# Kernel tuning notes

Measured on AMD Instinct MI355X. Metric: run time of the kernel, lower is better.

Reference implementation:

```python
import jax, jax.numpy as jnp
import numpy as np
import math

L, N, Q, C, H = 6, 32, 100, 256, 8


def setup_inputs() -> dict:
    key = jax.random.key(0)
    k0, k1, k2 = jax.random.split(key, 3)
    hs_pair = jax.random.normal(k0, (L, N, Q, C), jnp.float32)
    xb = math.sqrt(6.0 / (C + 3 * C))  # xavier_uniform bound for (3C, C)
    in_proj_w = jax.random.uniform(k1, (3 * C, C), jnp.float32, -xb, xb)
    in_proj_b = jnp.zeros((3 * C,), jnp.float32)
    ob = 1.0 / math.sqrt(C)  # nn.Linear default bound
    out_w = jax.random.uniform(k2, (C, C), jnp.float32, -ob, ob)
    out_b = jnp.zeros((C,), jnp.float32)
    return {"hs_pair": hs_pair, "in_proj_w": in_proj_w, "in_proj_b": in_proj_b,
            "out_w": out_w, "out_b": out_b}


def _smha(q, k, v, ipw, ipb, ow, ob, mask=None):
    """Sigmoid multi-head attention (SMHA), batch-first.
    q: (N,T,E), k/v: (N,S,E), mask: (T,S) bool (True = masked -> attn 0).
    Returns (out (N,T,E), head-averaged pre-normalization sigmoid weights (N,T,S))."""
    E = q.shape[-1]
    Dh = E // H
    Nb, T, _ = q.shape
    S = k.shape[1]
    wq, wk, wv = ipw[:E], ipw[E:2 * E], ipw[2 * E:]
    bq, bk, bv = ipb[:E], ipb[E:2 * E], ipb[2 * E:]
    qh = (q @ wq.T + bq).reshape(Nb, T, H, Dh)
    kh = (k @ wk.T + bk).reshape(Nb, S, H, Dh)
    vh = (v @ wv.T + bv).reshape(Nb, S, H, Dh)
    scores = jnp.einsum('nthd,nshd->nhts', qh, kh) / jnp.sqrt(jnp.asarray(Dh, qh.dtype))
    attn = jax.nn.sigmoid(scores)
    if mask is not None:
        attn = jnp.where(mask[None, None], 0.0, attn)  # sigmoid(-inf) == 0
    out = jnp.einsum('nhts,nshd->nthd', attn / (attn.sum(-1, keepdims=True) + 1e-4), vh)
    out = out.reshape(Nb, T, E) @ ow.T + ob
    return out, attn.mean(axis=1)


def _sqdist(a, b):
    # a (...,M,C), b (...,K,C) -> squared euclidean (...,M,K); avoids (M,K,C) diff tensor
    return jnp.maximum(jnp.sum(a * a, -1)[..., :, None] + jnp.sum(b * b, -1)[..., None, :]
                       - 2.0 * jnp.einsum('...mc,...kc->...mk', a, b), 0.0)


def _forward(hs_pair, ipw, ipb, ow, ob):
    hs = hs_pair[-1]  # (N,Q,C)
    Nb = hs.shape[0]

    # mean_farthest_assignment over all layers: centers (L,N,2,C)
    c1_all = hs_pair.mean(2, keepdims=True)                      # (L,N,1,C)
    d_all = _sqdist(c1_all, hs_pair)[..., 0, :]                  # (L,N,Q); sq dist preserves argmax
    far_all = jnp.argmax(d_all, -1)
    c2_all = jnp.take_along_axis(hs_pair, far_all[..., None, None], axis=2)
    centers = jnp.concatenate([c1_all, c2_all], 2)               # (L,N,2,C)

    # global field: 2 centers attend to Q pair features
    mf, assignment = _smha(centers[-1], hs, hs, ipw, ipb, ow, ob)  # (N,2,C), (N,2,Q)
    card = assignment.sum(-1)                                      # (N,2)
    s_idx = jnp.argmin(card, -1)
    d_idx = jnp.argmax(card, -1)
    cd = jnp.take_along_axis(mf, d_idx[:, None, None], 1)[:, 0]    # (N,C)
    cs = jnp.take_along_axis(mf, s_idx[:, None, None], 1)[:, 0]

    # base_idx row j = (j..j+Q-2) mod Q, i.e. it excludes (j-1) mod Q
    excl = (jnp.arange(Q) - 1) % Q
    sum_all = hs.sum(1)                                            # (N,C)
    rows = jnp.arange(Q)

    def branch(kv, c1):
        # kv (N,S,C); c1 (N,Q,C) leave-one-out means; returns shift (N,Q)
        S = kv.shape[1]
        d = _sqdist(c1, kv)                                        # (N,Q,S)
        em = jnp.arange(S)[None, :] == excl[:, None]               # exclude col (j-1)%Q
        far = jnp.argmax(jnp.where(em[None], -jnp.inf, d), -1)     # (N,Q)
        c2 = jnp.take_along_axis(kv, far[..., None], axis=1)       # (N,Q,C)
        cen = jnp.stack([c1, c2], 2).reshape(Nb, 2 * Q, C)         # interleaved [c1_j, c2_j]
        m = jnp.zeros((2 * Q, S), bool).at[2 * rows, rows].set(True).at[2 * rows + 1, rows].set(True)
        mfx, asg = _smha(cen, kv, kv, ipw, ipb, ow, ob, mask=m)    # (N,2Q,C), (N,2Q,S)
        mfx = mfx.reshape(Nb, Q, 2, C)
        asg = asg.reshape(Nb, Q, 2, S)
        cardx = asg.sum(-1)                                        # (N,Q,2)
        si = jnp.argmin(cardx, -1)
        di = jnp.argmax(cardx, -1)
        cdx = jnp.take_along_axis(mfx, di[..., None, None], 2)[:, :, 0]  # (N,Q,C)
        csx = jnp.take_along_axis(mfx, si[..., None, None], 2)[:, :, 0]
        return (jnp.sqrt(jnp.sum((cdx - cd[:, None]) ** 2, -1) + 1e-12)
                + jnp.sqrt(jnp.sum((csx - cs[:, None]) ** 2, -1) + 1e-12))

    # remove-one branch
    c1_rm = (sum_all[:, None] - hs[:, excl]) / (Q - 1)
    shift_rm = branch(hs, c1_rm)

    # mean-displace branch: subset + batch-mean pseudo point appended
    mean_pair = hs.mean(1, keepdims=True)                          # (N,1,C)
    kv_md = jnp.concatenate([hs, mean_pair], 1)                    # (N,Q+1,C)
    c1_md = (sum_all[:, None] - hs[:, excl] + mean_pair) / Q
    shift_md = branch(kv_md, c1_md)

    return assignment, s_idx, d_idx, shift_rm, shift_md


def reference(hs_pair, in_proj_w, in_proj_b, out_w, out_b):
    return _forward(hs_pair, in_proj_w, in_proj_b, out_w, out_b)
```

## Files before the change

### kernel.cpp

```cpp
#include <hip/hip_runtime.h>
#include <math.h>

#define NB 32
#define QQ 100
#define CC 256
#define HH 8
#define DH 32
#define SM 101
#define TT 200
#define TB 400
#define PW 768

typedef __attribute__((ext_vector_type(8))) short s16x8;
typedef __attribute__((ext_vector_type(4))) float f32x4;

__device__ inline ushort2 tsplit(float x) {
    unsigned u = __float_as_uint(x);
    float l = x - __uint_as_float(u & 0xffff0000u);
    ushort2 r;
    r.x = (unsigned short)(u >> 16);
    r.y = (unsigned short)(__float_as_uint(l) >> 16);
    return r;
}
__device__ inline unsigned short f2bf(float x) {
    unsigned u = __float_as_uint(x);
    return (unsigned short)((u + 0x7fffu + ((u >> 16) & 1u)) >> 16);
}

__global__ __launch_bounds__(256)
void meanrow_kernel(const float* __restrict__ hs, float* __restrict__ meanF) {
    int n = blockIdx.x, cb = blockIdx.y;
    int tid = threadIdx.x;
    int c = cb * 128 + (tid & 127), rh = tid >> 7;
    __shared__ float part[2][128];
    const float* h = hs + (size_t)n * QQ * CC;
    float s = 0.f;
    for (int q = rh * 50; q < rh * 50 + 50; ++q) s += h[(size_t)q * CC + c];
    part[rh][tid & 127] = s;
    __syncthreads();
    if (rh == 0) meanF[(size_t)n * CC + c] = (part[0][tid & 127] + part[1][tid & 127]) * 0.01f;
}

#define LDK 40
__global__ __launch_bounds__(256, 2)
void gemm_mfma(const float* __restrict__ hs, const float* __restrict__ meanF,
               const float* __restrict__ W_g, const float* __restrict__ bias,
               float* __restrict__ out, int M, int Nout) {
    __shared__ unsigned short Ahs[128][LDK], Als[128][LDK], Bhs[128][LDK], Bls[128][LDK];
    int tid = threadIdx.x;
    int lane = tid & 63, wave = tid >> 6;
    int wm = (wave >> 1) * 64, wn = (wave & 1) * 64;
    int fr = lane & 15, kb = lane >> 4;
    int bm = blockIdx.x * 128, bn = blockIdx.y * 128;
    int srow = tid >> 1, scol = (tid & 1) * 16;
    int am = bm + srow; if (am >= M) am = M - 1;
    int an = am / SM, ar = am - an * SM;
    const float* pA = (ar < QQ) ? hs + ((size_t)an * QQ + ar) * CC + scol
                                : meanF + (size_t)an * CC + scol;
    const float* pW = W_g + (size_t)(bn + srow) * CC + scol;
    f32x4 acc[4][4];
#pragma unroll
    for (int mi = 0; mi < 4; ++mi)
#pragma unroll
        for (int ni = 0; ni < 4; ++ni)
            acc[mi][ni] = (f32x4){0.f, 0.f, 0.f, 0.f};
    for (int k0 = 0; k0 < CC; k0 += 32) {
        float4 av[4], wv[4];
#pragma unroll
        for (int j = 0; j < 4; ++j) {
            av[j] = *(const float4*)(pA + k0 + 4 * j);
            wv[j] = *(const float4*)(pW + k0 + 4 * j);
        }
        __syncthreads();
#pragma unroll
        for (int j = 0; j < 4; ++j) {
            ushort2 sx = tsplit(av[j].x), sy = tsplit(av[j].y), sz = tsplit(av[j].z), sw = tsplit(av[j].w);
            ushort4 h4; h4.x = sx.x; h4.y = sy.x; h4.z = sz.x; h4.w = sw.x;
            ushort4 l4; l4.x = sx.y; l4.y = sy.y; l4.z = sz.y; l4.w = sw.y;
            *(ushort4*)&Ahs[srow][scol + 4 * j] = h4;
            *(ushort4*)&Als[srow][scol + 4 * j] = l4;
            ushort2 tx = tsplit(wv[j].x), ty = tsplit(wv[j].y), tz = tsplit(wv[j].z), tw = tsplit(wv[j].w);
            ushort4 wh4; wh4.x = tx.x; wh4.y = ty.x; wh4.z = tz.x; wh4.w = tw.x;
            ushort4 wl4; wl4.x = tx.y; wl4.y = ty.y; wl4.z = tz.y; wl4.w = tw.y;
            *(ushort4*)&Bhs[srow][scol + 4 * j] = wh4;
            *(ushort4*)&Bls[srow][scol + 4 * j] = wl4;
        }
        __syncthreads();
        s16x8 fah[4], fal[4], fbh[4], fbl[4];
#pragma unroll
        for (int mi = 0; mi < 4; ++mi) {
            fah[mi] = *(const s16x8*)&Ahs[wm + mi * 16 + fr][kb * 8];
            fal[mi] = *(const s16x8*)&Als[wm + mi * 16 + fr][kb * 8];
        }
#pragma unroll
        for (int ni = 0; ni < 4; ++ni) {
            fbh[ni] = *(const s16x8*)&Bhs[wn + ni * 16 + fr][kb * 8];
            fbl[ni] = *(const s16x8*)&Bls[wn + ni * 16 + fr][kb * 8];
        }
#pragma unroll
        for (int mi = 0; mi < 4; ++mi)
#pragma unroll
            for (int ni = 0; ni < 4; ++ni) {
                acc[mi][ni] = __builtin_amdgcn_mfma_f32_16x16x32_bf16(fah[mi], fbh[ni], acc[mi][ni], 0, 0, 0);
                acc[mi][ni] = __builtin_amdgcn_mfma_f32_16x16x32_bf16(fah[mi], fbl[ni], acc[mi][ni], 0, 0, 0);
                acc[mi][ni] = __builtin_amdgcn_mfma_f32_16x16x32_bf16(fal[mi], fbh[ni], acc[mi][ni], 0, 0, 0);
            }
    }
#pragma unroll
    for (int mi = 0; mi < 4; ++mi) {
        int mb = bm + wm + mi * 16 + kb * 4;
#pragma unroll
        for (int r = 0; r < 4; ++r) {
            int m = mb + r;
            if (m < M) {
#pragma unroll
                for (int ni = 0; ni < 4; ++ni) {
                    int col = bn + wn + ni * 16 + fr;
                    out[(size_t)m * Nout + col] = acc[mi][ni][r] + bias[col];
                }
            }
        }
    }
}

__global__ __launch_bounds__(256, 2)
void gram_strip(const float* __restrict__ hs, const float* __restrict__ meanF,
                float* __restrict__ G) {
    int ti = blockIdx.x, n = blockIdx.y;
    int tid = threadIdx.x;
    int wave = tid >> 6, lane = tid & 63;
    int fr = lane & 15, kb = lane >> 4;
    __shared__ unsigned short Ah[112][LDK], Al[112][LDK];
    const float* hb = hs + (size_t)n * QQ * CC;
    const float* mb = meanF + (size_t)n * CC;
    f32x4 acc[2];
    acc[0] = (f32x4){0.f, 0.f, 0.f, 0.f};
    acc[1] = (f32x4){0.f, 0.f, 0.f, 0.f};
    int tj0 = wave, tj1 = wave + 4;
    for (int k0 = 0; k0 < CC; k0 += 32) {
        __syncthreads();
        if (tid < 224) {
            int row = tid >> 1, kk = (tid & 1) * 16;
            float4 v[4];
            if (row < SM) {
                const float* rp = (row < QQ) ? hb + (size_t)row * CC : mb;
#pragma unroll
                for (int j = 0; j < 4; ++j) v[j] = *(const float4*)(rp + k0 + kk + 4 * j);
            } else {
#pragma unroll
                for (int j = 0; j < 4; ++j) v[j] = (float4){0.f, 0.f, 0.f, 0.f};
            }
#pragma unroll
            for (int j = 0; j < 4; ++j) {
                ushort2 sx = tsplit(v[j].x), sy = tsplit(v[j].y), sz = tsplit(v[j].z), sw = tsplit(v[j].w);
                ushort4 h4; h4.x = sx.x; h4.y = sy.x; h4.z = sz.x; h4.w = sw.x;
                ushort4 l4; l4.x = sx.y; l4.y = sy.y; l4.z = sz.y; l4.w = sw.y;
                *(ushort4*)&Ah[row][kk + 4 * j] = h4;
                *(ushort4*)&Al[row][kk + 4 * j] = l4;
            }
        }
        __syncthreads();
        s16x8 ah = *(const s16x8*)&Ah[ti * 16 + fr][kb * 8];
        s16x8 al = *(const s16x8*)&Al[ti * 16 + fr][kb * 8];
        {
            s16x8 bh = *(const s16x8*)&Ah[tj0 * 16 + fr][kb * 8];
            s16x8 bl = *(const s16x8*)&Al[tj0 * 16 + fr][kb * 8];
            acc[0] = __builtin_amdgcn_mfma_f32_16x16x32_bf16(ah, bh, acc[0], 0, 0, 0);
            acc[0] = __builtin_amdgcn_mfma_f32_16x16x32_bf16(ah, bl, acc[0], 0, 0, 0);
            acc[0] = __builtin_amdgcn_mfma_f32_16x16x32_bf16(al, bh, acc[0], 0, 0, 0);
        }
        if (tj1 < 7) {
            s16x8 bh = *(const s16x8*)&Ah[tj1 * 16 + fr][kb * 8];
            s16x8 bl = *(const s16x8*)&Al[tj1 * 16 + fr][kb * 8];
            acc[1] = __builtin_amdgcn_mfma_f32_16x16x32_bf16(ah, bh, acc[1], 0, 0, 0);
            acc[1] = __builtin_amdgcn_mfma_f32_16x16x32_bf16(ah, bl, acc[1], 0, 0, 0);
            acc[1] = __builtin_amdgcn_mfma_f32_16x16x32_bf16(al, bh, acc[1], 0, 0, 0);
        }
    }
    float* Gn = G + (size_t)n * SM * 104;
#pragma unroll
    for (int u = 0; u < 2; ++u) {
        int tj = u ? tj1 : tj0;
        if (tj >= 7) continue;
#pragma unroll
        for (int r = 0; r < 4; ++r) {
            int m = ti * 16 + kb * 4 + r;
            int col = tj * 16 + fr;
            if (m < SM && col < SM) Gn[(size_t)m * 104 + col] = (u ? acc[1] : acc[0])[r];
        }
    }
}

__global__ __launch_bounds__(256)
void farsel(const float* __restrict__ G, const float* __restrict__ P_all,
            float* __restrict__ Psum0, int* __restrict__ far0,
            int* __restrict__ far_rm, int* __restrict__ far_md) {
    int n = blockIdx.x;
    int tid = threadIdx.x;
    __shared__ float sumdot[104], meandot[104], norm[104];
    const float* Gn = G + (size_t)n * SM * 104;
    {
        const float* basep = P_all + (size_t)n * SM * PW + tid;
        float accp = 0.f;
        for (int q = 0; q < QQ; ++q) accp += basep[(size_t)q * PW];
        Psum0[(size_t)n * CC + tid] = accp;
    }
    if (tid < SM) {
        const float* row = Gn + (size_t)tid * 104;
        float a = 0.f;
        for (int q = 0; q < QQ; ++q) a += row[q];
        sumdot[tid] = a; meandot[tid] = row[QQ]; norm[tid] = row[tid];
    }
    __syncthreads();
    if (tid < QQ) {
        int q = tid, qm1 = (q + QQ - 1) % QQ;
        const float* gq = Gn + (size_t)qm1 * 104;
        int best = -1; float bv = -1e30f;
        for (int s = 0; s < QQ; ++s) {
            if (s == qm1) continue;
            float val = norm[s] - (sumdot[s] - gq[s]) * (2.f / 99.f);
            if (val > bv) { bv = val; best = s; }
        }
        far_rm[n * QQ + q] = best;
    } else if (tid >= 128 && tid < 128 + QQ) {
        int q = tid - 128, qm1 = (q + QQ - 1) % QQ;
        const float* gq = Gn + (size_t)qm1 * 104;
        int best = -1; float bv = -1e30f;
        for (int s = 0; s < SM; ++s) {
            if (s == qm1) continue;
            float val = norm[s] - (sumdot[s] - gq[s] + meandot[s]) * (2.f / 100.f);
            if (val > bv) { bv = val; best = s; }
        }
        far_md[n * QQ + q] = best;
    } else if (tid == 100) {
        int best = 0; float bv = -1e30f;
        for (int q = 0; q < QQ; ++q) {
            float val = norm[q] - 0.02f * sumdot[q];
            if (val > bv) { bv = val; best = q; }
        }
        far0[n] = best;
    }
}

__global__ __launch_bounds__(512)
void smhaB_kernel(const float* __restrict__ P_all, const int* __restrict__ far0,
                  const float* __restrict__ ow, const float* __restrict__ ob,
                  float* __restrict__ out_assign, float* __restrict__ out_sidx,
                  float* __restrict__ out_didx, float* __restrict__ cd,
                  float* __restrict__ cs) {
    int n = blockIdx.x;
    int tid = threadIdx.x;
    int h = tid >> 6, lane = tid & 63;
    __shared__ float at[HH][2][104];
    __shared__ float qsh[HH][2][DH];
    __shared__ float rsh[HH][2];
    __shared__ float pvs[2][CC];
    __shared__ int sdi[2];
    const float* base = P_all + (size_t)n * SM * PW;
    if (lane < 2 * DH) {
        int t = lane >> 5, d = lane & 31;
        int row = t ? far0[n] : QQ;
        qsh[h][t][d] = base[(size_t)row * PW + h * DH + d];
    }
    const float scl = 0.17677669529663687f;
    float p0 = 0.f, p1 = 0.f;
    for (int s = lane; s < 104; s += 64) {
        float a0v = 0.f, a1v = 0.f;
        if (s < QQ) {
            const float4* kr = (const float4*)(base + (size_t)s * PW + CC + h * DH);
            float d0 = 0.f, d1 = 0.f;
#pragma unroll
            for (int j = 0; j < 8; ++j) {
                float4 k4 = kr[j];
                d0 += qsh[h][0][4 * j] * k4.x + qsh[h][0][4 * j + 1] * k4.y
                    + qsh[h][0][4 * j + 2] * k4.z + qsh[h][0][4 * j + 3] * k4.w;
                d1 += qsh[h][1][4 * j] * k4.x + qsh[h][1][4 * j + 1] * k4.y
                    + qsh[h][1][4 * j + 2] * k4.z + qsh[h][1][4 * j + 3] * k4.w;
            }
            a0v = 1.f / (1.f + __expf(-d0 * scl));
            a1v = 1.f / (1.f + __expf(-d1 * scl));
            p0 += a0v; p1 += a1v;
        }
        at[h][0][s] = a0v;
        at[h][1][s] = a1v;
    }
#pragma unroll
    for (int off = 32; off > 0; off >>= 1) {
        p0 += __shfl_down(p0, off);
        p1 += __shfl_down(p1, off);
    }
    if (lane == 0) { rsh[h][0] = p0; rsh[h][1] = p1; }
    {
        int t = lane >> 5, d = lane & 31;
        float rv = (t ? p1 : p0);
        rv = __shfl(rv, 0);
        float inv = 1.f / (rv + 1e-4f);
        float acc = 0.f;
        const float* vb = base + 2 * CC + h * DH + d;
        for (int s = 0; s < QQ; ++s) acc += at[h][t][s] * vb[(size_t)s * PW];
        pvs[t][h * DH + d] = acc * inv;
    }
    __syncthreads();
    if (tid == 0) {
        float c0 = 0.f, c1v = 0.f;
        for (int h2 = 0; h2 < HH; ++h2) { c0 += rsh[h2][0]; c1v += rsh[h2][1]; }
        int si = (c1v < c0) ? 1 : 0;
        int di = (c1v > c0) ? 1 : 0;
        sdi[0] = si; sdi[1] = di;
        out_sidx[n] = (float)si;
        out_didx[n] = (float)di;
    }
    __syncthreads();
    if (tid < 2 * QQ) {
        int t = tid / QQ, s = tid % QQ;
        float m = 0.f;
#pragma unroll
        for (int h2 = 0; h2 < HH; ++h2) m += at[h2][t][s];
        out_assign[(size_t)n * 2 * QQ + tid] = m * 0.125f;
    }
    {
        int t = tid >> 8, c = tid & 255;
        const float4* wr4 = (const float4*)(ow + (size_t)c * CC);
        const float4* pz = (const float4*)&pvs[t][0];
        float a = ob[c];
#pragma unroll 8
        for (int k = 0; k < 64; ++k) {
            float4 w = wr4[k], x = pz[k];
            a += x.x * w.x + x.y * w.y + x.z * w.z + x.w * w.w;
        }
        if (t == sdi[1]) cd[(size_t)n * CC + c] = a;
        if (t == sdi[0]) cs[(size_t)n * CC + c] = a;
    }
}

__global__ __launch_bounds__(512)
void attn_mfma(const float* __restrict__ P_all, const float* __restrict__ Psum0,
               const int* __restrict__ far_rm, const int* __restrict__ far_md,
               float* __restrict__ pv, float* __restrict__ rowsum) {
    int h = blockIdx.x, n = blockIdx.y;
    int tid = threadIdx.x;
    int w = tid >> 6, lane = tid & 63;
    int fr = lane & 15, hi = lane >> 4;
    int d0 = hi * 8;
    __shared__ unsigned short Kh[112 * 40];
    __shared__ unsigned short Kl[112 * 40];
    __shared__ unsigned short Vt[32 * 136];
    __shared__ unsigned short Pb[8][64 * 40];
    __shared__ float rsL[8][64];
    const float* base = P_all + (size_t)n * SM * PW;
    for (int idx = tid; idx < 112 * 8; idx += 512) {
        int key = idx >> 3, d4 = (idx & 7) * 4;
        float4 kv = {0.f, 0.f, 0.f, 0.f}, vv = {0.f, 0.f, 0.f, 0.f};
        if (key < SM) {
            kv = *(const float4*)&base[(size_t)key * PW + CC + h * DH + d4];
            vv = *(const float4*)&base[(size_t)key * PW + 2 * CC + h * DH + d4];
        }
        ushort2 sx = tsplit(kv.x), sy = tsplit(kv.y), sz = tsplit(kv.z), sw = tsplit(kv.w);
        ushort4 h4; h4.x = sx.x; h4.y = sy.x; h4.z = sz.x; h4.w = sw.x;
        ushort4 l4; l4.x = sx.y; l4.y = sy.y; l4.z = sz.y; l4.w = sw.y;
        *(ushort4*)&Kh[key * 40 + d4] = h4;
        *(ushort4*)&Kl[key * 40 + d4] = l4;
        Vt[(d4 + 0) * 136 + key] = f2bf(vv.x);
        Vt[(d4 + 1) * 136 + key] = f2bf(vv.y);
        Vt[(d4 + 2) * 136 + key] = f2bf(vv.z);
        Vt[(d4 + 3) * 136 + key] = f2bf(vv.w);
    }
    for (int idx = tid; idx < 32 * 16; idx += 512) {
        int d = idx >> 4, key = 112 + (idx & 15);
        Vt[d * 136 + key] = 0;
    }
    __syncthreads();
    const float* Psum0n = Psum0 + n * CC;
    int rowbase = w * 50;
    unsigned short* Pw = Pb[w];
    const float scl = 0.17677669529663687f;
    s16x8 qh[4], ql[4];
    int mk[4], sb[4];
#pragma unroll
    for (int qi = 0; qi < 4; ++qi) {
        int lq = qi * 16 + fr;
        int row = rowbase + (lq < 50 ? lq : 49);
        int b = row >= TT;
        int t = row - b * TT;
        int q = t >> 1;
        mk[qi] = q; sb[qi] = b ? SM : QQ;
        float qv[8];
        if (t & 1) {
            int f = (b ? far_md : far_rm)[n * QQ + q];
            const float4* pr = (const float4*)(base + (size_t)f * PW + h * DH + d0);
            float4 v0 = pr[0], v1 = pr[1];
            qv[0] = v0.x; qv[1] = v0.y; qv[2] = v0.z; qv[3] = v0.w;
            qv[4] = v1.x; qv[5] = v1.y; qv[6] = v1.z; qv[7] = v1.w;
        } else {
            int qm1 = (q + QQ - 1) % QQ;
            const float4* ps = (const float4*)(Psum0n + h * DH + d0);
            const float4* pm = (const float4*)(base + (size_t)qm1 * PW + h * DH + d0);
            const float4* pmn = (const float4*)(base + (size_t)QQ * PW + h * DH + d0);
            float invd = b ? 0.01f : (1.f / 99.f);
            float bb = b ? 1.f : 0.f;
            float4 a0 = ps[0], c0 = pm[0], m0 = pmn[0];
            float4 a1 = ps[1], c1 = pm[1], m1 = pmn[1];
            qv[0] = (a0.x - c0.x + bb * m0.x) * invd;
            qv[1] = (a0.y - c0.y + bb * m0.y) * invd;
            qv[2] = (a0.z - c0.z + bb * m0.z) * invd;
            qv[3] = (a0.w - c0.w + bb * m0.w) * invd;
            qv[4] = (a1.x - c1.x + bb * m1.x) * invd;
            qv[5] = (a1.y - c1.y + bb * m1.y) * invd;
            qv[6] = (a1.z - c1.z + bb * m1.z) * invd;
            qv[7] = (a1.w - c1.w + bb * m1.w) * invd;
        }
        s16x8 qhv, qlv;
#pragma unroll
        for (int j = 0; j < 8; ++j) {
            ushort2 sp = tsplit(qv[j]);
            qhv[j] = (short)sp.x;
            qlv[j] = (short)sp.y;
        }
        qh[qi] = qhv; ql[qi] = qlv;
    }
    f32x4 pvacc[4][2];
#pragma unroll
    for (int qi = 0; qi < 4; ++qi) {
        pvacc[qi][0] = (f32x4){0.f, 0.f, 0.f, 0.f};
        pvacc[qi][1] = (f32x4){0.f, 0.f, 0.f, 0.f};
    }
    float rs[4] = {0.f, 0.f, 0.f, 0.f};
#pragma unroll
    for (int kc = 0; kc < 4; ++kc) {
        int k0 = kc * 32;
        {
            s16x8 ah = *(const s16x8*)&Kh[(k0 + fr) * 40 + d0];
            s16x8 al = *(const s16x8*)&Kl[(k0 + fr) * 40 + d0];
#pragma unroll
            for (int qi = 0; qi < 4; ++qi) {
                f32x4 s0 = (f32x4){0.f, 0.f, 0.f, 0.f};
                s0 = __builtin_amdgcn_mfma_f32_16x16x32_bf16(ah, qh[qi], s0, 0, 0, 0);
                s0 = __builtin_amdgcn_mfma_f32_16x16x32_bf16(ah, ql[qi], s0, 0, 0, 0);
                s0 = __builtin_amdgcn_mfma_f32_16x16x32_bf16(al, qh[qi], s0, 0, 0, 0);
                int kb0 = k0 + 4 * hi;
                float a0 = (kb0 + 0 < sb[qi] && kb0 + 0 != mk[qi]) ? 1.f / (1.f + __expf(-s0[0] * scl)) : 0.f;
                float a1 = (kb0 + 1 < sb[qi] && kb0 + 1 != mk[qi]) ? 1.f / (1.f + __expf(-s0[1] * scl)) : 0.f;
                float a2 = (kb0 + 2 < sb[qi] && kb0 + 2 != mk[qi]) ? 1.f / (1.f + __expf(-s0[2] * scl)) : 0.f;
                float a3 = (kb0 + 3 < sb[qi] && kb0 + 3 != mk[qi]) ? 1.f / (1.f + __expf(-s0[3] * scl)) : 0.f;
                rs[qi] += a0 + a1 + a2 + a3;
                ushort4 p4;
                p4.x = f2bf(a0); p4.y = f2bf(a1); p4.z = f2bf(a2); p4.w = f2bf(a3);
                *(ushort4*)&Pw[(qi * 16 + fr) * 40 + 4 * hi] = p4;
// ... 63 lines not shown
    }
}

__global__ __launch_bounds__(512)
void outshift(const float* __restrict__ pv, const float* __restrict__ ow,
              const float* __restrict__ ob, const float* __restrict__ cd,
              const float* __restrict__ cs, const float* __restrict__ rowsum,
              float* __restrict__ out_srm, float* __restrict__ out_smd) {
    __shared__ unsigned short Ahs[64][LDK], Als[64][LDK];
    __shared__ unsigned short Bhs[256][LDK], Bls[256][LDK];
    __shared__ float redcd[64][8], redcs[64][8];
    int tid = threadIdx.x;
    int lane = tid & 63, wave = tid >> 6;
    int wn = wave * 32;
    int fr = lane & 15, kb = lane >> 4;
    int bm = blockIdx.x * 64;
    int arow = tid >> 3, ak = (tid & 7) * 4;
    int brow = tid >> 1, bk = (tid & 1) * 16;
    const float* pA = pv + (size_t)(bm + arow) * CC + ak;
    const float* pB = ow + (size_t)brow * CC + bk;
    f32x4 acc[4][2];
#pragma unroll
    for (int mi = 0; mi < 4; ++mi)
#pragma unroll
        for (int ni = 0; ni < 2; ++ni)
            acc[mi][ni] = (f32x4){0.f, 0.f, 0.f, 0.f};
    for (int k0 = 0; k0 < CC; k0 += 32) {
        float4 av = *(const float4*)(pA + k0);
        float4 wv[4];
#pragma unroll
        for (int j = 0; j < 4; ++j) wv[j] = *(const float4*)(pB + k0 + 4 * j);
        __syncthreads();
        {
            ushort2 sx = tsplit(av.x), sy = tsplit(av.y), sz = tsplit(av.z), sw = tsplit(av.w);
            ushort4 h4; h4.x = sx.x; h4.y = sy.x; h4.z = sz.x; h4.w = sw.x;
            ushort4 l4; l4.x = sx.y; l4.y = sy.y; l4.z = sz.y; l4.w = sw.y;
            *(ushort4*)&Ahs[arow][ak] = h4;
            *(ushort4*)&Als[arow][ak] = l4;
        }
#pragma unroll
        for (int j = 0; j < 4; ++j) {
            ushort2 sx = tsplit(wv[j].x), sy = tsplit(wv[j].y), sz = tsplit(wv[j].z), sw = tsplit(wv[j].w);
            ushort4 h4; h4.x = sx.x; h4.y = sy.x; h4.z = sz.x; h4.w = sw.x;
            ushort4 l4; l4.x = sx.y; l4.y = sy.y; l4.z = sz.y; l4.w = sw.y;
            *(ushort4*)&Bhs[brow][bk + 4 * j] = h4;
            *(ushort4*)&Bls[brow][bk + 4 * j] = l4;
        }
        __syncthreads();
        s16x8 fah[4], fal[4], fbh[2], fbl[2];
#pragma unroll
        for (int mi = 0; mi < 4; ++mi) {
            fah[mi] = *(const s16x8*)&Ahs[mi * 16 + fr][kb * 8];
            fal[mi] = *(const s16x8*)&Als[mi * 16 + fr][kb * 8];
        }
#pragma unroll
        for (int ni = 0; ni < 2; ++ni) {
            fbh[ni] = *(const s16x8*)&Bhs[wn + ni * 16 + fr][kb * 8];
            fbl[ni] = *(const s16x8*)&Bls[wn + ni * 16 + fr][kb * 8];
        }
#pragma unroll
        for (int mi = 0; mi < 4; ++mi)
#pragma unroll
            for (int ni = 0; ni < 2; ++ni) {
                acc[mi][ni] = __builtin_amdgcn_mfma_f32_16x16x32_bf16(fah[mi], fbh[ni], acc[mi][ni], 0, 0, 0);
                acc[mi][ni] = __builtin_amdgcn_mfma_f32_16x16x32_bf16(fah[mi], fbl[ni], acc[mi][ni], 0, 0, 0);
                acc[mi][ni] = __builtin_amdgcn_mfma_f32_16x16x32_bf16(fal[mi], fbh[ni], acc[mi][ni], 0, 0, 0);
            }
    }
#pragma unroll
    for (int mi = 0; mi < 4; ++mi) {
#pragma unroll
        for (int r = 0; r < 4; ++r) {
            int lm = mi * 16 + kb * 4 + r;
            int g = bm + lm;
            int n = g / TB;
// ... 43 lines not shown

extern "C" void kernel_launch(void* const* d_in, const int* in_sizes, int n_in,
                              void* d_out, int out_size, void* d_ws, size_t ws_size,
                              hipStream_t stream) {
    const float* hs_pair = (const float*)d_in[0];
    const float* ipw = (const float*)d_in[1];
    const float* ipb = (const float*)d_in[2];
    const float* ow  = (const float*)d_in[3];
    const float* ob  = (const float*)d_in[4];
    const float* hs = hs_pair + (size_t)5 * NB * QQ * CC;

    float* ws = (float*)d_ws;
    size_t o = 0;
    float* meanF   = ws + o; o += NB * CC;
    float* P_all   = ws + o; o += (size_t)NB * SM * PW;
    float* Psum0   = ws + o; o += NB * CC;
    float* G       = ws + o; o += (size_t)NB * SM * 104;
    int*   far0    = (int*)(ws + o); o += NB;
    int*   far_rm  = (int*)(ws + o); o += NB * QQ;
    int*   far_md  = (int*)(ws + o); o += NB * QQ;
    float* cd      = ws + o; o += NB * CC;
    float* cs      = ws + o; o += NB * CC;
    float* pv      = ws + o; o += (size_t)NB * TB * CC;
    float* rowsum  = ws + o; o += (size_t)NB * HH * TB;
    if (o * sizeof(float) > ws_size) return;

    float* out = (float*)d_out;
    float* out_assign = out;
    float* out_sidx   = out + 6400;
    float* out_didx   = out + 6432;
    float* out_srm    = out + 6464;
    float* out_smd    = out + 9664;

    meanrow_kernel<<<dim3(NB, 2), 256, 0, stream>>>(hs, meanF);
    gemm_mfma<<<dim3((NB * SM + 127) / 128, PW / 128), 256, 0, stream>>>(
        hs, meanF, ipw, ipb, P_all, NB * SM, PW);
    gram_strip<<<dim3(7, NB), 256, 0, stream>>>(hs, meanF, G);
    farsel<<<NB, 256, 0, stream>>>(G, P_all, Psum0, far0, far_rm, far_md);
    smhaB_kernel<<<NB, 512, 0, stream>>>(P_all, far0, ow, ob, out_assign,
                                         out_sidx, out_didx, cd, cs);
    attn_mfma<<<dim3(HH, NB), 512, 0, stream>>>(P_all, Psum0, far_rm, far_md, pv, rowsum);
    outshift<<<NB * TB / 64, 512, 0, stream>>>(pv, ow, ob, cd, cs, rowsum, out_srm, out_smd);
}
```

Baseline: 116.8 us.

## Merge projection and Gram kernels, compute far0 in mean kernel, co-launch selection

The mean kernel now also computes the farthest point from the mean directly, so far0 no longer depends on the Gram matrix. The projection GEMM and Gram-strip kernels become one launch that dispatches on block index, and the far-point selection runs in the same launch as the SMHA-B block work. This cuts the launch count from seven to five and lets independent work run concurrently. The bf16 hi/lo split also switches from truncation to round-to-nearest, which changes numerics slightly.

```diff
diff --git a/kernel.cpp b/kernel.cpp
--- a/kernel.cpp
+++ b/kernel.cpp
@@ -14,322 +14,340 @@
 typedef __attribute__((ext_vector_type(8))) short s16x8;
 typedef __attribute__((ext_vector_type(4))) float f32x4;
 
-__device__ inline ushort2 tsplit(float x) {
-    unsigned u = __float_as_uint(x);
-    float l = x - __uint_as_float(u & 0xffff0000u);
-    ushort2 r;
-    r.x = (unsigned short)(u >> 16);
-    r.y = (unsigned short)(__float_as_uint(l) >> 16);
-    return r;
-}
 __device__ inline unsigned short f2bf(float x) {
     unsigned u = __float_as_uint(x);
     return (unsigned short)((u + 0x7fffu + ((u >> 16) & 1u)) >> 16);
 }
+__device__ inline float bf2f(unsigned short h) {
+    return __uint_as_float(((unsigned)h) << 16);
+}
+__device__ inline ushort2 rsplit(float x) {
+    ushort2 r;
+    r.x = f2bf(x);
+    r.y = f2bf(x - bf2f(r.x));
+    return r;
+}
 
 __global__ __launch_bounds__(256)
-void meanrow_kernel(const float* __restrict__ hs, float* __restrict__ meanF) {
-    int n = blockIdx.x, cb = blockIdx.y;
-    int tid = threadIdx.x;
-    int c = cb * 128 + (tid & 127), rh = tid >> 7;
-    __shared__ float part[2][128];
+void meanfar0(const float* __restrict__ hs, float* __restrict__ meanF,
+              int* __restrict__ far0) {
+    int n = blockIdx.x;
+    int c = threadIdx.x;
     const float* h = hs + (size_t)n * QQ * CC;
     float s = 0.f;
-    for (int q = rh * 50; q < rh * 50 + 50; ++q) s += h[(size_t)q * CC + c];
-    part[rh][tid & 127] = s;
+    for (int q = 0; q < QQ; ++q) s += h[q * CC + c];
+    float c1 = s * 0.01f;
+    meanF[(size_t)n * CC + c] = c1;
+    __shared__ float c1s[CC];
+    __shared__ float dls[QQ];
+    c1s[c] = c1;
     __syncthreads();
-    if (rh == 0) meanF[(size_t)n * CC + c] = (part[0][tid & 127] + part[1][tid & 127]) * 0.01f;
+    int wave = c >> 6, lane = c & 63;
+    for (int q = wave; q < QQ; q += 4) {
+        float p = 0.f;
+        for (int cc = lane; cc < CC; cc += 64) {
+            float d = c1s[cc] - h[q * CC + cc];
+            p += d * d;
+        }
+        for (int off = 32; off > 0; off >>= 1) p += __shfl_down(p, off);
+        if (lane == 0) dls[q] = p;
+    }
+    __syncthreads();
+    if (c == 0) {
+        int best = 0; float bv = dls[0];
+        for (int q = 1; q < QQ; ++q) if (dls[q] > bv) { bv = dls[q]; best = q; }
+        far0[n] = best;
+    }
 }
 
 #define LDK 40
+#define GEMM_BX 26
+#define GEMM_BY 6
+#define GEMM_NBLK (GEMM_BX * GEMM_BY)
 __global__ __launch_bounds__(256, 2)
-void gemm_mfma(const float* __restrict__ hs, const float* __restrict__ meanF,
-               const float* __restrict__ W_g, const float* __restrict__ bias,
-               float* __restrict__ out, int M, int Nout) {
-    __shared__ unsigned short Ahs[128][LDK], Als[128][LDK], Bhs[128][LDK], Bls[128][LDK];
+void projgram(const float* __restrict__ hs, const float* __restrict__ meanF,
+              const float* __restrict__ W_g, const float* __restrict__ bias,
+              float* __restrict__ out, float* __restrict__ G) {
+    __shared__ unsigned short u16buf[4 * 128 * LDK];
     int tid = threadIdx.x;
     int lane = tid & 63, wave = tid >> 6;
-    int wm = (wave >> 1) * 64, wn = (wave & 1) * 64;
     int fr = lane & 15, kb = lane >> 4;
-    int bm = blockIdx.x * 128, bn = blockIdx.y * 128;
-    int srow = tid >> 1, scol = (tid & 1) * 16;
-    int am = bm + srow; if (am >= M) am = M - 1;
-    int an = am / SM, ar = am - an * SM;
-    const float* pA = (ar < QQ) ? hs + ((size_t)an * QQ + ar) * CC + scol
-                                : meanF + (size_t)an * CC + scol;
-    const float* pW = W_g + (size_t)(bn + srow) * CC + scol;
-    f32x4 acc[4][4];
-#pragma unroll
-    for (int mi = 0; mi < 4; ++mi)
-#pragma unroll
-        for (int ni = 0; ni < 4; ++ni)
-            acc[mi][ni] = (f32x4){0.f, 0.f, 0.f, 0.f};
-    for (int k0 = 0; k0 < CC; k0 += 32) {
-        float4 av[4], wv[4];
-#pragma unroll
-        for (int j = 0; j < 4; ++j) {
-            av[j] = *(const float4*)(pA + k0 + 4 * j);
-            wv[j] = *(const float4*)(pW + k0 + 4 * j);
-        }
-        __syncthreads();
-#pragma unroll
-        for (int j = 0; j < 4; ++j) {
-            ushort2 sx = tsplit(av[j].x), sy = tsplit(av[j].y), sz = tsplit(av[j].z), sw = tsplit(av[j].w);
-            ushort4 h4; h4.x = sx.x; h4.y = sy.x; h4.z = sz.x; h4.w = sw.x;
-            ushort4 l4; l4.x = sx.y; l4.y = sy.y; l4.z = sz.y; l4.w = sw.y;
-            *(ushort4*)&Ahs[srow][scol + 4 * j] = h4;
-            *(ushort4*)&Als[srow][scol + 4 * j] = l4;
-            ushort2 tx = tsplit(wv[j].x), ty = tsplit(wv[j].y), tz = tsplit(wv[j].z), tw = tsplit(wv[j].w);
-            ushort4 wh4; wh4.x = tx.x; wh4.y = ty.x; wh4.z = tz.x; wh4.w = tw.x;
-            ushort4 wl4; wl4.x = tx.y; wl4.y = ty.y; wl4.z = tz.y; wl4.w = tw.y;
-            *(ushort4*)&Bhs[srow][scol + 4 * j] = wh4;
-            *(ushort4*)&Bls[srow][scol + 4 * j] = wl4;
-        }
-        __syncthreads();
-        s16x8 fah[4], fal[4], fbh[4], fbl[4];
-#pragma unroll
-        for (int mi = 0; mi < 4; ++mi) {
-            fah[mi] = *(const s16x8*)&Ahs[wm + mi * 16 + fr][kb * 8];
-            fal[mi] = *(const s16x8*)&Als[wm + mi * 16 + fr][kb * 8];
-        }
-#pragma unroll
-        for (int ni = 0; ni < 4; ++ni) {
-            fbh[ni] = *(const s16x8*)&Bhs[wn + ni * 16 + fr][kb * 8];
-            fbl[ni] = *(const s16x8*)&Bls[wn + ni * 16 + fr][kb * 8];
-        }
+    if (blockIdx.x < GEMM_NBLK) {
+        unsigned short* Ahs = u16buf;
+        unsigned short* Als = u16buf + 128 * LDK;
+        unsigned short* Bhs = u16buf + 2 * 128 * LDK;
+        unsigned short* Bls = u16buf + 3 * 128 * LDK;
+        const int M = NB * SM;
+        int bm = (blockIdx.x % GEMM_BX) * 128, bn = (blockIdx.x / GEMM_BX) * 128;
+        int wm = (wave >> 1) * 64, wn = (wave & 1) * 64;
+        int srow = tid >> 1, scol = (tid & 1) * 16;
+        int am = bm + srow; if (am >= M) am = M - 1;
+        int an = am / SM, ar = am - an * SM;
+        const float* pA = (ar < QQ) ? hs + ((size_t)an * QQ + ar) * CC + scol
+                                    : meanF + (size_t)an * CC + scol;
+        const float* pW = W_g + (size_t)(bn + srow) * CC + scol;
+        f32x4 acc[4][4];
 #pragma unroll
         for (int mi = 0; mi < 4; ++mi)
 #pragma unroll
-            for (int ni = 0; ni < 4; ++ni) {
-                acc[mi][ni] = __builtin_amdgcn_mfma_f32_16x16x32_bf16(fah[mi], fbh[ni], acc[mi][ni], 0, 0, 0);
-                acc[mi][ni] = __builtin_amdgcn_mfma_f32_16x16x32_bf16(fah[mi], fbl[ni], acc[mi][ni], 0, 0, 0);
-                acc[mi][ni] = __builtin_amdgcn_mfma_f32_16x16x32_bf16(fal[mi], fbh[ni], acc[mi][ni], 0, 0, 0);
-            }
-    }
-#pragma unroll
-    for (int mi = 0; mi < 4; ++mi) {
-        int mb = bm + wm + mi * 16 + kb * 4;
-#pragma unroll
-        for (int r = 0; r < 4; ++r) {
-            int m = mb + r;
-            if (m < M) {
-#pragma unroll
-                for (int ni = 0; ni < 4; ++ni) {
-                    int col = bn + wn + ni * 16 + fr;
-                    out[(size_t)m * Nout + col] = acc[mi][ni][r] + bias[col];
-                }
-            }
-        }
-    }
-}
-
-__global__ __launch_bounds__(256, 2)
-void gram_strip(const float* __restrict__ hs, const float* __restrict__ meanF,
-                float* __restrict__ G) {
-    int ti = blockIdx.x, n = blockIdx.y;
-    int tid = threadIdx.x;
-    int wave = tid >> 6, lane = tid & 63;
-    int fr = lane & 15, kb = lane >> 4;
-    __shared__ unsigned short Ah[112][LDK], Al[112][LDK];
-    const float* hb = hs + (size_t)n * QQ * CC;
-    const float* mb = meanF + (size_t)n * CC;
-    f32x4 acc[2];
-    acc[0] = (f32x4){0.f, 0.f, 0.f, 0.f};
-    acc[1] = (f32x4){0.f, 0.f, 0.f, 0.f};
-    int tj0 = wave, tj1 = wave + 4;
-    for (int k0 = 0; k0 < CC; k0 += 32) {
-        __syncthreads();
-        if (tid < 224) {
-            int row = tid >> 1, kk = (tid & 1) * 16;
-            float4 v[4];
-            if (row < SM) {
-                const float* rp = (row < QQ) ? hb + (size_t)row * CC : mb;
-#pragma unroll
-                for (int j = 0; j < 4; ++j) v[j] = *(const float4*)(rp + k0 + kk + 4 * j);
-            } else {
-#pragma unroll
-                for (int j = 0; j < 4; ++j) v[j] = (float4){0.f, 0.f, 0.f, 0.f};
-            }
+            for (int ni = 0; ni < 4; ++ni)
+                acc[mi][ni] = (f32x4){0.f, 0.f, 0.f, 0.f};
+        for (int k0 = 0; k0 < CC; k0 += 32) {
+            float4 av[4], wv[4];
 #pragma unroll
             for (int j = 0; j < 4; ++j) {
-                ushort2 sx = tsplit(v[j].x), sy = tsplit(v[j].y), sz = tsplit(v[j].z), sw = tsplit(v[j].w);
+                av[j] = *(const float4*)(pA + k0 + 4 * j);
+                wv[j] = *(const float4*)(pW + k0 + 4 * j);
+            }
+            __syncthreads();
+#pragma unroll
+            for (int j = 0; j < 4; ++j) {
+                ushort2 sx = rsplit(av[j].x), sy = rsplit(av[j].y), sz = rsplit(av[j].z), sw = rsplit(av[j].w);
                 ushort4 h4; h4.x = sx.x; h4.y = sy.x; h4.z = sz.x; h4.w = sw.x;
                 ushort4 l4; l4.x = sx.y; l4.y = sy.y; l4.z = sz.y; l4.w = sw.y;
-                *(ushort4*)&Ah[row][kk + 4 * j] = h4;
-                *(ushort4*)&Al[row][kk + 4 * j] = l4;
-            }
+                *(ushort4*)&Ahs[srow * LDK + scol + 4 * j] = h4;
+                *(ushort4*)&Als[srow * LDK + scol + 4 * j] = l4;
+                ushort2 tx = rsplit(wv[j].x), ty = rsplit(wv[j].y), tz = rsplit(wv[j].z), tw = rsplit(wv[j].w);
+                ushort4 wh4; wh4.x = tx.x; wh4.y = ty.x; wh4.z = tz.x; wh4.w = tw.x;
+                ushort4 wl4; wl4.x = tx.y; wl4.y = ty.y; wl4.z = tz.y; wl4.w = tw.y;
+                *(ushort4*)&Bhs[srow * LDK + scol + 4 * j] = wh4;
+                *(ushort4*)&Bls[srow * LDK + scol + 4 * j] = wl4;
+            }
+            __syncthreads();
+            s16x8 fah[4], fal[4], fbh[4], fbl[4];
+#pragma unroll
+            for (int mi = 0; mi < 4; ++mi) {
+                fah[mi] = *(const s16x8*)&Ahs[(wm + mi * 16 + fr) * LDK + kb * 8];
+                fal[mi] = *(const s16x8*)&Als[(wm + mi * 16 + fr) * LDK + kb * 8];
+            }
+#pragma unroll
+            for (int ni = 0; ni < 4; ++ni) {
+                fbh[ni] = *(const s16x8*)&Bhs[(wn + ni * 16 + fr) * LDK + kb * 8];
+                fbl[ni] = *(const s16x8*)&Bls[(wn + ni * 16 + fr) * LDK + kb * 8];
+            }
+#pragma unroll
+            for (int mi = 0; mi < 4; ++mi)
+#pragma unroll
+                for (int ni = 0; ni < 4; ++ni) {
+                    acc[mi][ni] = __builtin_amdgcn_mfma_f32_16x16x32_bf16(fah[mi], fbh[ni], acc[mi][ni], 0, 0, 0);
+                    acc[mi][ni] = __builtin_amdgcn_mfma_f32_16x16x32_bf16(fah[mi], fbl[ni], acc[mi][ni], 0, 0, 0);
+                    acc[mi][ni] = __builtin_amdgcn_mfma_f32_16x16x32_bf16(fal[mi], fbh[ni], acc[mi][ni], 0, 0, 0);
+                }
+        }
+#pragma unroll
+        for (int mi = 0; mi < 4; ++mi) {
+            int mb = bm + wm + mi * 16 + kb * 4;
+#pragma unroll
+            for (int r = 0; r < 4; ++r) {
+                int m = mb + r;
+                if (m < M) {
+#pragma unroll
+                    for (int ni = 0; ni < 4; ++ni) {
+                        int col = bn + wn + ni * 16 + fr;
+                        out[(size_t)m * PW + col] = acc[mi][ni][r] + bias[col];
+                    }
+                }
+            }
+        }
+    } else {
+        int bi = blockIdx.x - GEMM_NBLK;
+        int ti = bi % 7, n = bi / 7;
+        unsigned short* Ah = u16buf;
+        unsigned short* Al = u16buf + 112 * LDK;
+        const float* hb = hs + (size_t)n * QQ * CC;
+        const float* mb = meanF + (size_t)n * CC;
+        f32x4 acc[2];
+        acc[0] = (f32x4){0.f, 0.f, 0.f, 0.f};
+        acc[1] = (f32x4){0.f, 0.f, 0.f, 0.f};
+        int tj0 = wave, tj1 = wave + 4;
+        for (int k0 = 0; k0 < CC; k0 += 32) {
+            __syncthreads();
+            if (tid < 224) {
+                int row = tid >> 1, kk = (tid & 1) * 16;
+                float4 v[4];
+                if (row < SM) {
+                    const float* rp = (row < QQ) ? hb + (size_t)row * CC : mb;
+#pragma unroll
+                    for (int j = 0; j < 4; ++j) v[j] = *(const float4*)(rp + k0 + kk + 4 * j);
+                } else {
+#pragma unroll
+                    for (int j = 0; j < 4; ++j) v[j] = (float4){0.f, 0.f, 0.f, 0.f};
+                }
+#pragma unroll
+                for (int j = 0; j < 4; ++j) {
+                    ushort2 sx = rsplit(v[j].x), sy = rsplit(v[j].y), sz = rsplit(v[j].z), sw = rsplit(v[j].w);
+                    ushort4 h4; h4.x = sx.x; h4.y = sy.x; h4.z = sz.x; h4.w = sw.x;
+                    ushort4 l4; l4.x = sx.y; l4.y = sy.y; l4.z = sz.y; l4.w = sw.y;
+                    *(ushort4*)&Ah[row * LDK + kk + 4 * j] = h4;
+                    *(ushort4*)&Al[row * LDK + kk + 4 * j] = l4;
+                }
+            }
+            __syncthreads();
+            s16x8 ah = *(const s16x8*)&Ah[(ti * 16 + fr) * LDK + kb * 8];
+            s16x8 al = *(const s16x8*)&Al[(ti * 16 + fr) * LDK + kb * 8];
+            {
+                s16x8 bh = *(const s16x8*)&Ah[(tj0 * 16 + fr) * LDK + kb * 8];
+                s16x8 bl = *(const s16x8*)&Al[(tj0 * 16 + fr) * LDK + kb * 8];
+                acc[0] = __builtin_amdgcn_mfma_f32_16x16x32_bf16(ah, bh, acc[0], 0, 0, 0);
+                acc[0] = __builtin_amdgcn_mfma_f32_16x16x32_bf16(ah, bl, acc[0], 0, 0, 0);
+                acc[0] = __builtin_amdgcn_mfma_f32_16x16x32_bf16(al, bh, acc[0], 0, 0, 0);
+            }
+            if (tj1 < 7) {
+                s16x8 bh = *(const s16x8*)&Ah[(tj1 * 16 + fr) * LDK + kb * 8];
+                s16x8 bl = *(const s16x8*)&Al[(tj1 * 16 + fr) * LDK + kb * 8];
+                acc[1] = __builtin_amdgcn_mfma_f32_16x16x32_bf16(ah, bh, acc[1], 0, 0, 0);
+                acc[1] = __builtin_amdgcn_mfma_f32_16x16x32_bf16(ah, bl, acc[1], 0, 0, 0);
+                acc[1] = __builtin_amdgcn_mfma_f32_16x16x32_bf16(al, bh, acc[1], 0, 0, 0);
+            }
+        }
+        float* Gn = G + (size_t)n * SM * 104;
+#pragma unroll
+        for (int u = 0; u < 2; ++u) {
+            int tj = u ? tj1 : tj0;
+            if (tj >= 7) continue;
+#pragma unroll
+            for (int r = 0; r < 4; ++r) {
+                int m = ti * 16 + kb * 4 + r;
+                int col = tj * 16 + fr;
+                if (m < SM && col < SM) Gn[(size_t)m * 104 + col] = (u ? acc[1] : acc[0])[r];
+            }
+        }
+    }
+}
+
+__global__ __launch_bounds__(512)
+void selB(const float* __restrict__ G, const float* __restrict__ P_all,
+          const int* __restrict__ far0, const float* __restrict__ ow,
+          const float* __restrict__ ob, float* __restrict__ Psum0,
+          int* __restrict__ far_rm, int* __restrict__ far_md,
+          float* __restrict__ out_assign, float* __restrict__ out_sidx,
+          float* __restrict__ out_didx, float* __restrict__ cd,
+          float* __restrict__ cs) {
+    int tid = threadIdx.x;
+    if (blockIdx.x < NB) {
+        int n = blockIdx.x;
+        __shared__ float sumdot[104], meandot[104], norm[104];
+        __shared__ float psumP[2][CC];
+        const float* Gn = G + (size_t)n * SM * 104;
+        {
+            int c = tid & 255, half = tid >> 8;
+            const float* basep = P_all + (size_t)n * SM * PW + c;
+            float accp = 0.f;
+            for (int q = half * 50; q < half * 50 + 50; ++q) accp += basep[(size_t)q * PW];
+            psumP[half][c] = accp;
+        }
+        if (tid < SM) {
+            const float* row = Gn + (size_t)tid * 104;
+            float a = 0.f;
+            for (int q = 0; q < QQ; ++q) a += row[q];
+            sumdot[tid] = a; meandot[tid] = row[QQ]; norm[tid] = row[tid];
         }
         __syncthreads();
-        s16x8 ah = *(const s16x8*)&Ah[ti * 16 + fr][kb * 8];
-        s16x8 al = *(const s16x8*)&Al[ti * 16 + fr][kb * 8];
+        if (tid < 256) Psum0[(size_t)n * CC + tid] = psumP[0][tid] + psumP[1][tid];
+        if (tid < QQ) {
+            int q = tid, qm1 = (q + QQ - 1) % QQ;
+            const float* gq = Gn + (size_t)qm1 * 104;
+            int best = -1; float bv = -1e30f;
+            for (int s = 0; s < QQ; ++s) {
+                if (s == qm1) continue;
+                float val = norm[s] - (sumdot[s] - gq[s]) * (2.f / 99.f);
+                if (val > bv) { bv = val; best = s; }
+            }
+            far_rm[n * QQ + q] = best;
+        } else if (tid >= 128 && tid < 128 + QQ) {
+            int q = tid - 128, qm1 = (q + QQ - 1) % QQ;
+            const float* gq = Gn + (size_t)qm1 * 104;
+            int best = -1; float bv = -1e30f;
+            for (int s = 0; s < SM; ++s) {
+                if (s == qm1) continue;
+                float val = norm[s] - (sumdot[s] - gq[s] + meandot[s]) * (2.f / 100.f);
+                if (val > bv) { bv = val; best = s; }
+            }
+            far_md[n * QQ + q] = best;
+        }
+    } else {
+        int n = blockIdx.x - NB;
+        int h = tid >> 6, lane = tid & 63;
+        __shared__ float at[HH][2][104];
+        __shared__ float qsh[HH][2][DH];
+        __shared__ float rsh[HH][2];
+        __shared__ float pvs[2][CC];
+        __shared__ int sdi[2];
+        const float* base = P_all + (size_t)n * SM * PW;
+        if (lane < 2 * DH) {
+            int t = lane >> 5, d = lane & 31;
+            int row = t ? far0[n] : QQ;
+            qsh[h][t][d] = base[(size_t)row * PW + h * DH + d];
+        }
+        const float scl = 0.17677669529663687f;
+        float p0 = 0.f, p1 = 0.f;
+        for (int s = lane; s < 104; s += 64) {
+            float a0v = 0.f, a1v = 0.f;
+            if (s < QQ) {
+                const float4* kr = (const float4*)(base + (size_t)s * PW + CC + h * DH);
+                float d0 = 0.f, d1 = 0.f;
+#pragma unroll
+                for (int j = 0; j < 8; ++j) {
+                    float4 k4 = kr[j];
+                    d0 += qsh[h][0][4 * j] * k4.x + qsh[h][0][4 * j + 1] * k4.y
+                        + qsh[h][0][4 * j + 2] * k4.z + qsh[h][0][4 * j + 3] * k4.w;
+                    d1 += qsh[h][1][4 * j] * k4.x + qsh[h][1][4 * j + 1] * k4.y
+                        + qsh[h][1][4 * j + 2] * k4.z + qsh[h][1][4 * j + 3] * k4.w;
+                }
+                a0v = 1.f / (1.f + __expf(-d0 * scl));
+                a1v = 1.f / (1.f + __expf(-d1 * scl));
+                p0 += a0v; p1 += a1v;
+            }
+            at[h][0][s] = a0v;
+            at[h][1][s] = a1v;
+        }
+#pragma unroll
+        for (int off = 32; off > 0; off >>= 1) {
+            p0 += __shfl_down(p0, off);
+            p1 += __shfl_down(p1, off);
+        }
+        if (lane == 0) { rsh[h][0] = p0; rsh[h][1] = p1; }
         {
-            s16x8 bh = *(const s16x8*)&Ah[tj0 * 16 + fr][kb * 8];
-            s16x8 bl = *(const s16x8*)&Al[tj0 * 16 + fr][kb * 8];
-            acc[0] = __builtin_amdgcn_mfma_f32_16x16x32_bf16(ah, bh, acc[0], 0, 0, 0);
-            acc[0] = __builtin_amdgcn_mfma_f32_16x16x32_bf16(ah, bl, acc[0], 0, 0, 0);
-            acc[0] = __builtin_amdgcn_mfma_f32_16x16x32_bf16(al, bh, acc[0], 0, 0, 0);
-        }
-        if (tj1 < 7) {
-            s16x8 bh = *(const s16x8*)&Ah[tj1 * 16 + fr][kb * 8];
-            s16x8 bl = *(const s16x8*)&Al[tj1 * 16 + fr][kb * 8];
-            acc[1] = __builtin_amdgcn_mfma_f32_16x16x32_bf16(ah, bh, acc[1], 0, 0, 0);
-            acc[1] = __builtin_amdgcn_mfma_f32_16x16x32_bf16(ah, bl, acc[1], 0, 0, 0);
-            acc[1] = __builtin_amdgcn_mfma_f32_16x16x32_bf16(al, bh, acc[1], 0, 0, 0);
-        }
-    }
-    float* Gn = G + (size_t)n * SM * 104;
-#pragma unroll
-    for (int u = 0; u < 2; ++u) {
-        int tj = u ? tj1 : tj0;
-        if (tj >= 7) continue;
-#pragma unroll
-        for (int r = 0; r < 4; ++r) {
-            int m = ti * 16 + kb * 4 + r;
-            int col = tj * 16 + fr;
-            if (m < SM && col < SM) Gn[(size_t)m * 104 + col] = (u ? acc[1] : acc[0])[r];
-        }
-    }
-}
-
-__global__ __launch_bounds__(256)
-void farsel(const float* __restrict__ G, const float* __restrict__ P_all,
-            float* __restrict__ Psum0, int* __restrict__ far0,
-            int* __restrict__ far_rm, int* __restrict__ far_md) {
-    int n = blockIdx.x;
-    int tid = threadIdx.x;
-    __shared__ float sumdot[104], meandot[104], norm[104];
-    const float* Gn = G + (size_t)n * SM * 104;
-    {
-        const float* basep = P_all + (size_t)n * SM * PW + tid;
-        float accp = 0.f;
-        for (int q = 0; q < QQ; ++q) accp += basep[(size_t)q * PW];
-        Psum0[(size_t)n * CC + tid] = accp;
-    }
-    if (tid < SM) {
-        const float* row = Gn + (size_t)tid * 104;
-        float a = 0.f;
-        for (int q = 0; q < QQ; ++q) a += row[q];
-        sumdot[tid] = a; meandot[tid] = row[QQ]; norm[tid] = row[tid];
-    }
-    __syncthreads();
-    if (tid < QQ) {
-        int q = tid, qm1 = (q + QQ - 1) % QQ;
-        const float* gq = Gn + (size_t)qm1 * 104;
-        int best = -1; float bv = -1e30f;
-        for (int s = 0; s < QQ; ++s) {
-            if (s == qm1) continue;
-            float val = norm[s] - (sumdot[s] - gq[s]) * (2.f / 99.f);
-            if (val > bv) { bv = val; best = s; }
-        }
-        far_rm[n * QQ + q] = best;
-    } else if (tid >= 128 && tid < 128 + QQ) {
-        int q = tid - 128, qm1 = (q + QQ - 1) % QQ;
-        const float* gq = Gn + (size_t)qm1 * 104;
-        int best = -1; float bv = -1e30f;
-        for (int s = 0; s < SM; ++s) {
-            if (s == qm1) continue;
-            float val = norm[s] - (sumdot[s] - gq[s] + meandot[s]) * (2.f / 100.f);
-            if (val > bv) { bv = val; best = s; }
-        }
-        far_md[n * QQ + q] = best;
-    } else if (tid == 100) {
-        int best = 0; float bv = -1e30f;
-        for (int q = 0; q < QQ; ++q) {
-            float val = norm[q] - 0.02f * sumdot[q];
-            if (val > bv) { bv = val; best = q; }
-        }
-        far0[n] = best;
-    }
-}
-
-__global__ __launch_bounds__(512)
-void smhaB_kernel(const float* __restrict__ P_all, const int* __restrict__ far0,
-                  const float* __restrict__ ow, const float* __restrict__ ob,
-                  float* __restrict__ out_assign, float* __restrict__ out_sidx,
-                  float* __restrict__ out_didx, float* __restrict__ cd,
-                  float* __restrict__ cs) {
-    int n = blockIdx.x;
-    int tid = threadIdx.x;
-    int h = tid >> 6, lane = tid & 63;
-    __shared__ float at[HH][2][104];
-    __shared__ float qsh[HH][2][DH];
-    __shared__ float rsh[HH][2];
-    __shared__ float pvs[2][CC];
-    __shared__ int sdi[2];
-    const float* base = P_all + (size_t)n * SM * PW;
-    if (lane < 2 * DH) {
-        int t = lane >> 5, d = lane & 31;
-        int row = t ? far0[n] : QQ;
-        qsh[h][t][d] = base[(size_t)row * PW + h * DH + d];
-    }
-    const float scl = 0.17677669529663687f;
-    float p0 = 0.f, p1 = 0.f;
-    for (int s = lane; s < 104; s += 64) {
-        float a0v = 0.f, a1v = 0.f;
-        if (s < QQ) {
-            const float4* kr = (const float4*)(base + (size_t)s * PW + CC + h * DH);
-            float d0 = 0.f, d1 = 0.f;
-#pragma unroll
-            for (int j = 0; j < 8; ++j) {
-                float4 k4 = kr[j];
-                d0 += qsh[h][0][4 * j] * k4.x + qsh[h][0][4 * j + 1] * k4.y
-                    + qsh[h][0][4 * j + 2] * k4.z + qsh[h][0][4 * j + 3] * k4.w;
-                d1 += qsh[h][1][4 * j] * k4.x + qsh[h][1][4 * j + 1] * k4.y
-                    + qsh[h][1][4 * j + 2] * k4.z + qsh[h][1][4 * j + 3] * k4.w;
-            }
-            a0v = 1.f / (1.f + __expf(-d0 * scl));
-            a1v = 1.f / (1.f + __expf(-d1 * scl));
-            p0 += a0v; p1 += a1v;
-        }
-        at[h][0][s] = a0v;
-        at[h][1][s] = a1v;
-    }
-#pragma unroll
-    for (int off = 32; off > 0; off >>= 1) {
-        p0 += __shfl_down(p0, off);
-        p1 += __shfl_down(p1, off);
-    }
-    if (lane == 0) { rsh[h][0] = p0; rsh[h][1] = p1; }
-    {
-        int t = lane >> 5, d = lane & 31;
-        float rv = (t ? p1 : p0);
-        rv = __shfl(rv, 0);
-        float inv = 1.f / (rv + 1e-4f);
-        float acc = 0.f;
-        const float* vb = base + 2 * CC + h * DH + d;
-        for (int s = 0; s < QQ; ++s) acc += at[h][t][s] * vb[(size_t)s * PW];
-        pvs[t][h * DH + d] = acc * inv;
-    }
-    __syncthreads();
-    if (tid == 0) {
-        float c0 = 0.f, c1v = 0.f;
-        for (int h2 = 0; h2 < HH; ++h2) { c0 += rsh[h2][0]; c1v += rsh[h2][1]; }
-        int si = (c1v < c0) ? 1 : 0;
-        int di = (c1v > c0) ? 1 : 0;
-        sdi[0] = si; sdi[1] = di;
-        out_sidx[n] = (float)si;
-        out_didx[n] = (float)di;
-    }
-    __syncthreads();
-    if (tid < 2 * QQ) {
-        int t = tid / QQ, s = tid % QQ;
-        float m = 0.f;
-#pragma unroll
-        for (int h2 = 0; h2 < HH; ++h2) m += at[h2][t][s];
-        out_assign[(size_t)n * 2 * QQ + tid] = m * 0.125f;
-    }
-    {
-        int t = tid >> 8, c = tid & 255;
-        const float4* wr4 = (const float4*)(ow + (size_t)c * CC);
-        const float4* pz = (const float4*)&pvs[t][0];
-        float a = ob[c];
+            int t = lane >> 5, d = lane & 31;
+            float rv = (t ? p1 : p0);
+            rv = __shfl(rv, 0);
+            float inv = 1.f / (rv + 1e-4f);
+            float acc = 0.f;
+            const float* vb = base + 2 * CC + h * DH + d;
+            for (int s = 0; s < QQ; ++s) acc += at[h][t][s] * vb[(size_t)s * PW];
+            pvs[t][h * DH + d] = acc * inv;
+        }
+        __syncthreads();
+        if (tid == 0) {
+            float c0 = 0.f, c1v = 0.f;
+            for (int h2 = 0; h2 < HH; ++h2) { c0 += rsh[h2][0]; c1v += rsh[h2][1]; }
+            int si = (c1v < c0) ? 1 : 0;
+            int di = (c1v > c0) ? 1 : 0;
+            sdi[0] = si; sdi[1] = di;
+            out_sidx[n] = (float)si;
+            out_didx[n] = (float)di;
+        }
+        __syncthreads();
+        if (tid < 2 * QQ) {
+            int t = tid / QQ, s = tid % QQ;
+            float m = 0.f;
+#pragma unroll
+            for (int h2 = 0; h2 < HH; ++h2) m += at[h2][t][s];
+            out_assign[(size_t)n * 2 * QQ + tid] = m * 0.125f;
+        }
+        {
+            int t = tid >> 8, c = tid & 255;
+            const float4* wr4 = (const float4*)(ow + (size_t)c * CC);
+            const float4* pz = (const float4*)&pvs[t][0];
+            float a = ob[c];
 #pragma unroll 8
-        for (int k = 0; k < 64; ++k) {
-            float4 w = wr4[k], x = pz[k];
-            a += x.x * w.x + x.y * w.y + x.z * w.z + x.w * w.w;
-        }
-        if (t == sdi[1]) cd[(size_t)n * CC + c] = a;
-        if (t == sdi[0]) cs[(size_t)n * CC + c] = a;
+            for (int k = 0; k < 64; ++k) {
+                float4 w = wr4[k], x = pz[k];
+                a += x.x * w.x + x.y * w.y + x.z * w.z + x.w * w.w;
+            }
+            if (t == sdi[1]) cd[(size_t)n * CC + c] = a;
+            if (t == sdi[0]) cs[(size_t)n * CC + c] = a;
+        }
     }
 }
 
@@ -355,7 +373,7 @@
             kv = *(const float4*)&base[(size_t)key * PW + CC + h * DH + d4];
             vv = *(const float4*)&base[(size_t)key * PW + 2 * CC + h * DH + d4];
         }
-        ushort2 sx = tsplit(kv.x), sy = tsplit(kv.y), sz = tsplit(kv.z), sw = tsplit(kv.w);
+        ushort2 sx = rsplit(kv.x), sy = rsplit(kv.y), sz = rsplit(kv.z), sw = rsplit(kv.w);
         ushort4 h4; h4.x = sx.x; h4.y = sy.x; h4.z = sz.x; h4.w = sw.x;
         ushort4 l4; l4.x = sx.y; l4.y = sy.y; l4.z = sz.y; l4.w = sw.y;
         *(ushort4*)&Kh[key * 40 + d4] = h4;
@@ -412,7 +430,7 @@
         s16x8 qhv, qlv;
 #pragma unroll
         for (int j = 0; j < 8; ++j) {
-            ushort2 sp = tsplit(qv[j]);
+            ushort2 sp = rsplit(qv[j]);
             qhv[j] = (short)sp.x;
             qlv[j] = (short)sp.y;
         }
@@ -542,7 +560,7 @@
         for (int j = 0; j < 4; ++j) wv[j] = *(const float4*)(pB + k0 + 4 * j);
         __syncthreads();
         {
-            ushort2 sx = tsplit(av.x), sy = tsplit(av.y), sz = tsplit(av.z), sw = tsplit(av.w);
+            ushort2 sx = rsplit(av.x), sy = rsplit(av.y), sz = rsplit(av.z), sw = rsplit(av.w);
             ushort4 h4; h4.x = sx.x; h4.y = sy.x; h4.z = sz.x; h4.w = sw.x;
             ushort4 l4; l4.x = sx.y; l4.y = sy.y; l4.z = sz.y; l4.w = sw.y;
             *(ushort4*)&Ahs[arow][ak] = h4;
@@ -550,7 +568,7 @@
         }
 #pragma unroll
         for (int j = 0; j < 4; ++j) {
-            ushort2 sx = tsplit(wv[j].x), sy = tsplit(wv[j].y), sz = tsplit(wv[j].z), sw = tsplit(wv[j].w);
+            ushort2 sx = rsplit(wv[j].x), sy = rsplit(wv[j].y), sz = rsplit(wv[j].z), sw = rsplit(wv[j].w);
             ushort4 h4; h4.x = sx.x; h4.y = sy.x; h4.z = sz.x; h4.w = sw.x;
             ushort4 l4; l4.x = sx.y; l4.y = sy.y; l4.z = sz.y; l4.w = sw.y;
             *(ushort4*)&Bhs[brow][bk + 4 * j] = h4;
@@ -660,13 +678,10 @@
     float* out_srm    = out + 6464;
     float* out_smd    = out + 9664;
 
-    meanrow_kernel<<<dim3(NB, 2), 256, 0, stream>>>(hs, meanF);
-    gemm_mfma<<<dim3((NB * SM + 127) / 128, PW / 128), 256, 0, stream>>>(
-        hs, meanF, ipw, ipb, P_all, NB * SM, PW);
-    gram_strip<<<dim3(7, NB), 256, 0, stream>>>(hs, meanF, G);
-    farsel<<<NB, 256, 0, stream>>>(G, P_all, Psum0, far0, far_rm, far_md);
-    smhaB_kernel<<<NB, 512, 0, stream>>>(P_all, far0, ow, ob, out_assign,
-                                         out_sidx, out_didx, cd, cs);
+    meanfar0<<<NB, 256, 0, stream>>>(hs, meanF, far0);
+    projgram<<<GEMM_NBLK + 7 * NB, 256, 0, stream>>>(hs, meanF, ipw, ipb, P_all, G);
+    selB<<<2 * NB, 512, 0, stream>>>(G, P_all, far0, ow, ob, Psum0, far_rm, far_md,
+                                     out_assign, out_sidx, out_didx, cd, cs);
     attn_mfma<<<dim3(HH, NB), 512, 0, stream>>>(P_all, Psum0, far_rm, far_md, pv, rowsum);
     outshift<<<NB * TB / 64, 512, 0, stream>>>(pv, ow, ob, cd, cs, rowsum, out_srm, out_smd);
 }
```

Result: faster. 110.6 us (-5.4%).
